# Performance work log

Hardware: AMD Instinct MI355X
Metric: run time of the kernel (lower is better)

Reference implementation:

```python
import jax, jax.numpy as jnp
import numpy as np

N = 20000        # nodes
E = 320000       # edges (avg degree 16)
IN = 128         # in_channels
D = 64           # out_channels == per-head dim (PyG TransformerConv)
H = 4            # heads
EPS_BN = 1e-5


def setup_inputs() -> dict:
    key = jax.random.key(0)
    ks = jax.random.split(key, 12)
    x = jax.random.normal(ks[0], (N, IN), jnp.float32)
    edge_index = jax.random.randint(ks[1], (2, E), 0, N, dtype=jnp.int64)
    s = 1.0 / np.sqrt(IN)
    Wq = jax.random.normal(ks[2], (IN, H * D), jnp.float32) * s
    bq = jnp.zeros((H * D,), jnp.float32)
    Wk = jax.random.normal(ks[3], (IN, H * D), jnp.float32) * s
    bk = jnp.zeros((H * D,), jnp.float32)
    Wv = jax.random.normal(ks[4], (IN, H * D), jnp.float32) * s
    bv = jnp.zeros((H * D,), jnp.float32)
    Wskip = jax.random.normal(ks[5], (IN, D), jnp.float32) * s
    bskip = jnp.zeros((D,), jnp.float32)
    gamma = jnp.ones((D,), jnp.float32)
    beta = jnp.zeros((D,), jnp.float32)
    return {"x": x, "edge_index": edge_index, "Wq": Wq, "bq": bq,
            "Wk": Wk, "bk": bk, "Wv": Wv, "bv": bv,
            "Wskip": Wskip, "bskip": bskip, "gamma": gamma, "beta": beta}


def reference(x, edge_index, Wq, bq, Wk, bk, Wv, bv, Wskip, bskip, gamma, beta):
    src = edge_index[0]   # message source j
    dst = edge_index[1]   # message target i
    # node-level projections, [N, H, D]
    q = (x @ Wq + bq).reshape(N, H, D)
    k = (x @ Wk + bk).reshape(N, H, D)
    v = (x @ Wv + bv).reshape(N, H, D)
    # per-edge attention logits [E, H]
    scores = jnp.einsum('ehd,ehd->eh', q[dst], k[src]) / jnp.sqrt(jnp.float32(D))
    # segment softmax over incoming edges of each target node
    smax = jax.ops.segment_max(scores, dst, num_segments=N)
    smax = jnp.where(jnp.isfinite(smax), smax, 0.0)  # isolated nodes
    p = jnp.exp(scores - smax[dst])
    denom = jax.ops.segment_sum(p, dst, num_segments=N)
    alpha = p / (denom[dst] + 1e-16)                  # [E, H]
    # scatter-aggregate messages: [N, H, D]
    msg = jax.ops.segment_sum(alpha[:, :, None] * v[src], dst, num_segments=N)
    # concat=False -> mean over heads; root skip connection
    out = msg.mean(axis=1) + x @ Wskip + bskip        # [N, D]
    # BatchNorm1d over nodes (training-mode batch stats, biased var)
    mu = out.mean(axis=0)
    var = out.var(axis=0)
    out = (out - mu) * jax.lax.rsqrt(var + EPS_BN) * gamma + beta
    # exact (erf) GELU, dropout = identity at eval
    return jax.nn.gelu(out, approximate=False)
```

## Files before the change

### kernel.cpp

```cpp
#include <hip/hip_runtime.h>
#include <hip/hip_fp16.h>
#include <math.h>

#define NNODES 20000
#define NEDGES 320000
#define CIN 128
#define DOUT 64
#define NHEAD 4
#define HD 256
#define PROJW 320
#define KVW 512

__global__ __launch_bounds__(256) void proj_kernel(
    const float* __restrict__ x,
    const float* __restrict__ Wq, const float* __restrict__ bq,
    const float* __restrict__ Wk, const float* __restrict__ bk,
    const float* __restrict__ Wv, const float* __restrict__ bv,
    const float* __restrict__ Ws, const float* __restrict__ bs,
    float* __restrict__ proj, __half* __restrict__ kvh)
{
    __shared__ float Ast[32][68];
    __shared__ float Bs[32][68];
    const int tile_n = blockIdx.x;
    const float* W; const float* bias; int segw; int lc0;
    if (tile_n < 4)       { W = Wq; bias = bq; segw = HD;   lc0 = tile_n * 64; }
    else if (tile_n < 8)  { W = Wk; bias = bk; segw = HD;   lc0 = (tile_n - 4) * 64; }
    else if (tile_n < 12) { W = Wv; bias = bv; segw = HD;   lc0 = (tile_n - 8) * 64; }
    else                  { W = Ws; bias = bs; segw = DOUT; lc0 = 0; }
    const int row0 = blockIdx.y * 64;
    const int tid = threadIdx.x;
    const int tx = tid & 15, ty = tid >> 4;

    float acc[4][4] = {};
    for (int k0 = 0; k0 < CIN; k0 += 32) {
        #pragma unroll
        for (int l = 0; l < 2; ++l) {
            int idx = tid + l * 256;
            int r = idx >> 3, c4 = (idx & 7) << 2;
            int gr = row0 + r;
            float4 v = make_float4(0.f, 0.f, 0.f, 0.f);
            if (gr < NNODES)
                v = *reinterpret_cast<const float4*>(x + (size_t)gr * CIN + k0 + c4);
            Ast[c4 + 0][r] = v.x; Ast[c4 + 1][r] = v.y;
            Ast[c4 + 2][r] = v.z; Ast[c4 + 3][r] = v.w;
        }
        #pragma unroll
        for (int l = 0; l < 2; ++l) {
            int idx = tid + l * 256;
            int r = idx >> 4, c4 = (idx & 15) << 2;
            float4 v = *reinterpret_cast<const float4*>(W + (size_t)(k0 + r) * segw + lc0 + c4);
            *reinterpret_cast<float4*>(&Bs[r][c4]) = v;
        }
        __syncthreads();
        #pragma unroll
        for (int kk = 0; kk < 32; ++kk) {
            const float4 a = *reinterpret_cast<const float4*>(&Ast[kk][ty * 4]);
            const float4 b = *reinterpret_cast<const float4*>(&Bs[kk][tx * 4]);
            acc[0][0] += a.x * b.x; acc[0][1] += a.x * b.y; acc[0][2] += a.x * b.z; acc[0][3] += a.x * b.w;
            acc[1][0] += a.y * b.x; acc[1][1] += a.y * b.y; acc[1][2] += a.y * b.z; acc[1][3] += a.y * b.w;
            acc[2][0] += a.z * b.x; acc[2][1] += a.z * b.y; acc[2][2] += a.z * b.z; acc[2][3] += a.z * b.w;
            acc[3][0] += a.w * b.x; acc[3][1] += a.w * b.y; acc[3][2] += a.w * b.z; acc[3][3] += a.w * b.w;
        }
        __syncthreads();
    }
    #pragma unroll
    for (int i = 0; i < 4; ++i) {
        int gr = row0 + ty * 4 + i;
        if (gr >= NNODES) continue;
        float4 o;
        o.x = acc[i][0] + bias[lc0 + tx * 4 + 0];
        o.y = acc[i][1] + bias[lc0 + tx * 4 + 1];
        o.z = acc[i][2] + bias[lc0 + tx * 4 + 2];
        o.w = acc[i][3] + bias[lc0 + tx * 4 + 3];
        if (tile_n < 4) {
            *reinterpret_cast<float4*>(proj + (size_t)gr * PROJW + tile_n * 64 + tx * 4) = o;
        } else if (tile_n < 12) {
            int col = (tile_n < 8) ? (tile_n - 4) * 64 + tx * 4
                                   : 256 + (tile_n - 8) * 64 + tx * 4;
            __half2 h0 = __floats2half2_rn(o.x, o.y);
            __half2 h1 = __floats2half2_rn(o.z, o.w);
            __half2* dst = reinterpret_cast<__half2*>(kvh + (size_t)gr * KVW + col);
            dst[0] = h0; dst[1] = h1;
        } else {
            *reinterpret_cast<float4*>(proj + (size_t)gr * PROJW + 256 + tx * 4) = o;
        }
    }
}

__global__ void hist_kernel(const int* __restrict__ ei, int* __restrict__ deg)
{
    int e = blockIdx.x * blockDim.x + threadIdx.x;
    if (e >= NEDGES) return;
    atomicAdd(&deg[ei[NEDGES + e]], 1);
}

__global__ __launch_bounds__(1024) void scan_kernel(
    const int* __restrict__ deg, int* __restrict__ rowptr, int* __restrict__ cursor)
{
    __shared__ int sd[1024];
    const int t = threadIdx.x;
    const int chunk = 20;
    const int base = t * chunk;
    int tsum = 0;
    for (int i = 0; i < chunk; ++i) {
        int idx = base + i;
        tsum += (idx < NNODES) ? deg[idx] : 0;
    }
    sd[t] = tsum; __syncthreads();
    for (int off = 1; off < 1024; off <<= 1) {
        int v = (t >= off) ? sd[t - off] : 0;
        __syncthreads();
        sd[t] += v;
        __syncthreads();
    }
    int run = sd[t] - tsum;
    for (int i = 0; i < chunk; ++i) {
        int idx = base + i;
        if (idx < NNODES) {
            int d = deg[idx];
            rowptr[idx] = run; cursor[idx] = run;
            run += d;
        }
    }
    if (t == 1023) rowptr[NNODES] = sd[1023];
}

__global__ void scatter_kernel(const int* __restrict__ ei, int* __restrict__ cursor,
                               int* __restrict__ col)
{
    int e = blockIdx.x * blockDim.x + threadIdx.x;
    if (e >= NEDGES) return;
    int src = ei[e];
    int dst = ei[NEDGES + e];
    int pos = atomicAdd(&cursor[dst], 1);
    col[pos] = src;
}

__global__ __launch_bounds__(256) void attn_kernel(
    const float* __restrict__ proj, const __half* __restrict__ kvh,
    const int* __restrict__ rowptr, const int* __restrict__ col,
    float* __restrict__ out_pre)
{
    const int node = blockIdx.x * 4 + (threadIdx.x >> 6);
    if (node >= NNODES) return;
    const int lane = threadIdx.x & 63;
    const int lane4 = lane * 4;

    const float4 q = *reinterpret_cast<const float4*>(proj + (size_t)node * PROJW + lane4);

    float m = -INFINITY, l = 0.f;
    float ax = 0.f, ay = 0.f, az = 0.f, aw = 0.f;
    int p = rowptr[node];
    const int pend = rowptr[node + 1];

    int j = (p < pend) ? col[p] : 0;
    const __half* bj = kvh + (size_t)j * KVW + lane4;
    uint2 kraw = *reinterpret_cast<const uint2*>(bj);
    uint2 vraw = *reinterpret_cast<const uint2*>(bj + 256);

    for (; p < pend; ++p) {
        const int p1 = p + 1;
        const int jn = (p1 < pend) ? col[p1] : j;
        const __half* bn = kvh + (size_t)jn * KVW + lane4;
        const uint2 krawn = *reinterpret_cast<const uint2*>(bn);
        const uint2 vrawn = *reinterpret_cast<const uint2*>(bn + 256);

        const float2 k0 = __half22float2(*reinterpret_cast<const __half2*>(&kraw.x));
        const float2 k1 = __half22float2(*reinterpret_cast<const __half2*>(&kraw.y));
        float partial = q.x * k0.x + q.y * k0.y + q.z * k1.x + q.w * k1.y;
        partial += __shfl_xor(partial, 1, 16);
        partial += __shfl_xor(partial, 2, 16);
        partial += __shfl_xor(partial, 4, 16);
        partial += __shfl_xor(partial, 8, 16);
        const float s = partial * 0.125f;
        const float mnew = fmaxf(m, s);
        const float scale = __expf(m - mnew);
        const float pc = __expf(s - mnew);
        const float2 v0 = __half22float2(*reinterpret_cast<const __half2*>(&vraw.x));
        const float2 v1 = __half22float2(*reinterpret_cast<const __half2*>(&vraw.y));
        l = l * scale + pc;
        ax = ax * scale + pc * v0.x;
        ay = ay * scale + pc * v0.y;
        az = az * scale + pc * v1.x;
        aw = aw * scale + pc * v1.y;
        m = mnew;
        kraw = krawn; vraw = vrawn;
    }
    const float inv = 1.f / (l + 1e-16f);
    float rx = ax * inv, ry = ay * inv, rz = az * inv, rw = aw * inv;
    rx += __shfl_xor(rx, 16); rx += __shfl_xor(rx, 32);
    ry += __shfl_xor(ry, 16); ry += __shfl_xor(ry, 32);
    rz += __shfl_xor(rz, 16); rz += __shfl_xor(rz, 32);
    rw += __shfl_xor(rw, 16); rw += __shfl_xor(rw, 32);
    if (lane < 16) {
        const float4 sk = *reinterpret_cast<const float4*>(proj + (size_t)node * PROJW + 256 + lane4);
        float4 o;
        o.x = rx * 0.25f + sk.x;
        o.y = ry * 0.25f + sk.y;
        o.z = rz * 0.25f + sk.z;
        o.w = rw * 0.25f + sk.w;
        *reinterpret_cast<float4*>(out_pre + (size_t)node * DOUT + lane4) = o;
    }
}

__global__ __launch_bounds__(256) void bnred_kernel(
    const float* __restrict__ out_pre, float* __restrict__ bnacc)
{
    const int tid = threadIdx.x;
    const int c = tid & 63, g = tid >> 6;
    float s = 0.f, ss = 0.f;
    for (int r = blockIdx.x * 4 + g; r < NNODES; r += gridDim.x * 4) {
        float v = out_pre[(size_t)r * DOUT + c];
        s += v; ss += v * v;
    }
    __shared__ float sd[256];
    sd[tid] = s; __syncthreads();
    float s4 = 0.f;
    if (g == 0) s4 = sd[tid] + sd[tid + 64] + sd[tid + 128] + sd[tid + 192];
    __syncthreads();
    sd[tid] = ss; __syncthreads();
    if (g == 0) {
        float ss4 = sd[tid] + sd[tid + 64] + sd[tid + 128] + sd[tid + 192];
        atomicAdd(&bnacc[c], s4);
        atomicAdd(&bnacc[64 + c], ss4);
    }
}

__global__ __launch_bounds__(256) void final_kernel(
    const float* __restrict__ out_pre, const float* __restrict__ bnacc,
    const float* __restrict__ gamma, const float* __restrict__ beta,
    float* __restrict__ out)
{
    int idx = blockIdx.x * blockDim.x + threadIdx.x;
    if (idx >= NNODES * DOUT) return;
    const int c = idx & 63;
    const float mu = bnacc[c] * (1.f / NNODES);
    const float var = bnacc[64 + c] * (1.f / NNODES) - mu * mu;
    float v = (out_pre[idx] - mu) * rsqrtf(var + 1e-5f) * gamma[c] + beta[c];
    out[idx] = v * 0.5f * (1.f + erff(v * 0.70710678118654752f));
}

extern "C" void kernel_launch(void* const* d_in, const int* in_sizes, int n_in,
                              void* d_out, int out_size, void* d_ws, size_t ws_size,
                              hipStream_t stream) {
    const float* x     = (const float*)d_in[0];
    const int*   ei    = (const int*)d_in[1];
    const float* Wq    = (const float*)d_in[2];
    const float* bq    = (const float*)d_in[3];
    const float* Wk    = (const float*)d_in[4];
    const float* bk    = (const float*)d_in[5];
    const float* Wv    = (const float*)d_in[6];
    const float* bv    = (const float*)d_in[7];
    const float* Wskip = (const float*)d_in[8];
    const float* bskip = (const float*)d_in[9];
    const float* gamma = (const float*)d_in[10];
    const float* beta  = (const float*)d_in[11];
    float* out = (float*)d_out;

    __half* kvh     = (__half*)d_ws;
    float*  proj    = (float*)((char*)d_ws + (size_t)NNODES * KVW * sizeof(__half));
    float*  out_pre = proj + (size_t)NNODES * PROJW;
    float*  bnacc   = out_pre + (size_t)NNODES * DOUT;
    int*    deg     = (int*)(bnacc + 128);
    int*    rowptr  = deg + NNODES;
    int*    cursor  = rowptr + NNODES + 1;
    int*    col     = cursor + NNODES;

    hipMemsetAsync(bnacc, 0, (128 + NNODES) * sizeof(int), stream);

    proj_kernel<<<dim3(13, (NNODES + 63) / 64), 256, 0, stream>>>(
        x, Wq, bq, Wk, bk, Wv, bv, Wskip, bskip, proj, kvh);
    hist_kernel<<<(NEDGES + 255) / 256, 256, 0, stream>>>(ei, deg);
    scan_kernel<<<1, 1024, 0, stream>>>(deg, rowptr, cursor);
    scatter_kernel<<<(NEDGES + 255) / 256, 256, 0, stream>>>(ei, cursor, col);
    attn_kernel<<<NNODES / 4, 256, 0, stream>>>(proj, kvh, rowptr, col, out_pre);
    bnred_kernel<<<128, 256, 0, stream>>>(out_pre, bnacc);
    final_kernel<<<(NNODES * DOUT + 255) / 256, 256, 0, stream>>>(
        out_pre, bnacc, gamma, beta, out);
}
```

Baseline: 277.7 us.

## Replace FP32 SIMT projection GEMM with FP16 MFMA wave-level GEMM

Adds a prep kernel that converts x to fp16 and transposes and concatenates the four weight matrices into one fp16 column-major buffer plus a combined bias. A new projection kernel has each wave compute a 16x64 output tile with mfma_f32_16x16x32_f16, replacing the LDS-tiled FP32 FMA GEMM. This moves the projection onto the matrix cores, at the cost of an extra launch, extra global traffic for the conversion, fp16 rounding of the inputs, and narrower strided scalar output stores.

```diff
diff --git a/kernel.cpp b/kernel.cpp
--- a/kernel.cpp
+++ b/kernel.cpp
@@ -10,79 +10,103 @@
 #define HD 256
 #define PROJW 320
 #define KVW 512
-
-__global__ __launch_bounds__(256) void proj_kernel(
+#define NCOL 832
+#define NWAVES (1250 * 13)
+
+typedef __attribute__((ext_vector_type(8))) _Float16 half8;
+typedef __attribute__((ext_vector_type(4))) float f32x4;
+
+__global__ __launch_bounds__(256) void prep_kernel(
     const float* __restrict__ x,
     const float* __restrict__ Wq, const float* __restrict__ bq,
     const float* __restrict__ Wk, const float* __restrict__ bk,
     const float* __restrict__ Wv, const float* __restrict__ bv,
     const float* __restrict__ Ws, const float* __restrict__ bs,
+    _Float16* __restrict__ xh, _Float16* __restrict__ Wth,
+    float* __restrict__ bias832)
+{
+    int i = blockIdx.x * 256 + threadIdx.x;
+    if (i < NNODES * CIN / 8) {
+        const float4* xv = reinterpret_cast<const float4*>(x);
+        float4 u = xv[2 * i], v = xv[2 * i + 1];
+        half8 h = { (_Float16)u.x, (_Float16)u.y, (_Float16)u.z, (_Float16)u.w,
+                    (_Float16)v.x, (_Float16)v.y, (_Float16)v.z, (_Float16)v.w };
+        *reinterpret_cast<half8*>(xh + (size_t)i * 8) = h;
+        return;
+    }
+    i -= NNODES * CIN / 8;
+    if (i < NCOL * CIN) {
+        int c = i >> 7, k = i & 127;
+        float v;
+        if (c < 256)      v = Wq[k * HD + c];
+        else if (c < 512) v = Wk[k * HD + (c - 256)];
+        else if (c < 768) v = Wv[k * HD + (c - 512)];
+        else              v = Ws[k * DOUT + (c - 768)];
+        Wth[(size_t)c * CIN + k] = (_Float16)v;
+        return;
+    }
+    i -= NCOL * CIN;
+    if (i < NCOL) {
+        float v;
+        if (i < 256)      v = bq[i];
+        else if (i < 512) v = bk[i - 256];
+        else if (i < 768) v = bv[i - 512];
+        else              v = bs[i - 768];
+        bias832[i] = v;
+    }
+}
+
+__global__ __launch_bounds__(256) void wproj_kernel(
+    const _Float16* __restrict__ xh, const _Float16* __restrict__ Wth,
+    const float* __restrict__ bias832,
     float* __restrict__ proj, __half* __restrict__ kvh)
 {
-    __shared__ float Ast[32][68];
-    __shared__ float Bs[32][68];
-    const int tile_n = blockIdx.x;
-    const float* W; const float* bias; int segw; int lc0;
-    if (tile_n < 4)       { W = Wq; bias = bq; segw = HD;   lc0 = tile_n * 64; }
-    else if (tile_n < 8)  { W = Wk; bias = bk; segw = HD;   lc0 = (tile_n - 4) * 64; }
-    else if (tile_n < 12) { W = Wv; bias = bv; segw = HD;   lc0 = (tile_n - 8) * 64; }
-    else                  { W = Ws; bias = bs; segw = DOUT; lc0 = 0; }
-    const int row0 = blockIdx.y * 64;
-    const int tid = threadIdx.x;
-    const int tx = tid & 15, ty = tid >> 4;
-
-    float acc[4][4] = {};
-    for (int k0 = 0; k0 < CIN; k0 += 32) {
-        #pragma unroll
-        for (int l = 0; l < 2; ++l) {
-            int idx = tid + l * 256;
-            int r = idx >> 3, c4 = (idx & 7) << 2;
-            int gr = row0 + r;
-            float4 v = make_float4(0.f, 0.f, 0.f, 0.f);
-            if (gr < NNODES)
-                v = *reinterpret_cast<const float4*>(x + (size_t)gr * CIN + k0 + c4);
-            Ast[c4 + 0][r] = v.x; Ast[c4 + 1][r] = v.y;
-            Ast[c4 + 2][r] = v.z; Ast[c4 + 3][r] = v.w;
-        }
-        #pragma unroll
-        for (int l = 0; l < 2; ++l) {
-            int idx = tid + l * 256;
-            int r = idx >> 4, c4 = (idx & 15) << 2;
-            float4 v = *reinterpret_cast<const float4*>(W + (size_t)(k0 + r) * segw + lc0 + c4);
-            *reinterpret_cast<float4*>(&Bs[r][c4]) = v;
-        }
-        __syncthreads();
-        #pragma unroll
-        for (int kk = 0; kk < 32; ++kk) {
-            const float4 a = *reinterpret_cast<const float4*>(&Ast[kk][ty * 4]);
-            const float4 b = *reinterpret_cast<const float4*>(&Bs[kk][tx * 4]);
-            acc[0][0] += a.x * b.x; acc[0][1] += a.x * b.y; acc[0][2] += a.x * b.z; acc[0][3] += a.x * b.w;
-            acc[1][0] += a.y * b.x; acc[1][1] += a.y * b.y; acc[1][2] += a.y * b.z; acc[1][3] += a.y * b.w;
-            acc[2][0] += a.z * b.x; acc[2][1] += a.z * b.y; acc[2][2] += a.z * b.z; acc[2][3] += a.z * b.w;
-            acc[3][0] += a.w * b.x; acc[3][1] += a.w * b.y; acc[3][2] += a.w * b.z; acc[3][3] += a.w * b.w;
-        }
-        __syncthreads();
-    }
+    const int wv = blockIdx.x * 4 + (threadIdx.x >> 6);
+    if (wv >= NWAVES) return;
+    const int l = threadIdx.x & 63;
+    const int ct = wv / 1250, rt = wv % 1250;
+    const int row0 = rt * 16, colb = ct * 64;
+    const int lrow = l & 15, lk8 = (l >> 4) * 8;
+
+    const _Float16* xr = xh + (size_t)(row0 + lrow) * CIN + lk8;
+    const half8 a0 = *reinterpret_cast<const half8*>(xr);
+    const half8 a1 = *reinterpret_cast<const half8*>(xr + 32);
+    const half8 a2 = *reinterpret_cast<const half8*>(xr + 64);
+    const half8 a3 = *reinterpret_cast<const half8*>(xr + 96);
+
+    f32x4 acc[4];
     #pragma unroll
-    for (int i = 0; i < 4; ++i) {
-        int gr = row0 + ty * 4 + i;
-        if (gr >= NNODES) continue;
-        float4 o;
-        o.x = acc[i][0] + bias[lc0 + tx * 4 + 0];
-        o.y = acc[i][1] + bias[lc0 + tx * 4 + 1];
-        o.z = acc[i][2] + bias[lc0 + tx * 4 + 2];
-        o.w = acc[i][3] + bias[lc0 + tx * 4 + 3];
-        if (tile_n < 4) {
-            *reinterpret_cast<float4*>(proj + (size_t)gr * PROJW + tile_n * 64 + tx * 4) = o;
-        } else if (tile_n < 12) {
-            int col = (tile_n < 8) ? (tile_n - 4) * 64 + tx * 4
-                                   : 256 + (tile_n - 8) * 64 + tx * 4;
-            __half2 h0 = __floats2half2_rn(o.x, o.y);
-            __half2 h1 = __floats2half2_rn(o.z, o.w);
-            __half2* dst = reinterpret_cast<__half2*>(kvh + (size_t)gr * KVW + col);
-            dst[0] = h0; dst[1] = h1;
+    for (int cg = 0; cg < 4; ++cg) {
+        const _Float16* wr = Wth + (size_t)(colb + cg * 16 + lrow) * CIN + lk8;
+        const half8 b0 = *reinterpret_cast<const half8*>(wr);
+        const half8 b1 = *reinterpret_cast<const half8*>(wr + 32);
+        const half8 b2 = *reinterpret_cast<const half8*>(wr + 64);
+        const half8 b3 = *reinterpret_cast<const half8*>(wr + 96);
+        f32x4 c = {0.f, 0.f, 0.f, 0.f};
+        c = __builtin_amdgcn_mfma_f32_16x16x32_f16(a0, b0, c, 0, 0, 0);
+        c = __builtin_amdgcn_mfma_f32_16x16x32_f16(a1, b1, c, 0, 0, 0);
+        c = __builtin_amdgcn_mfma_f32_16x16x32_f16(a2, b2, c, 0, 0, 0);
+        c = __builtin_amdgcn_mfma_f32_16x16x32_f16(a3, b3, c, 0, 0, 0);
+        acc[cg] = c;
+    }
+
+    const int orow = row0 + (l >> 4) * 4;
+    #pragma unroll
+    for (int cg = 0; cg < 4; ++cg) {
+        const int c = colb + cg * 16 + lrow;
+        const float bias = bias832[c];
+        if (ct < 4) {
+            #pragma unroll
+            for (int r = 0; r < 4; ++r)
+                proj[(size_t)(orow + r) * PROJW + c] = acc[cg][r] + bias;
+        } else if (ct < 12) {
+            #pragma unroll
+            for (int r = 0; r < 4; ++r)
+                kvh[(size_t)(orow + r) * KVW + (c - 256)] = __float2half(acc[cg][r] + bias);
         } else {
-            *reinterpret_cast<float4*>(proj + (size_t)gr * PROJW + 256 + tx * 4) = o;
+            #pragma unroll
+            for (int r = 0; r < 4; ++r)
+                proj[(size_t)(orow + r) * PROJW + (c - 512)] = acc[cg][r] + bias;
         }
     }
 }
@@ -257,19 +281,24 @@
     const float* beta  = (const float*)d_in[11];
     float* out = (float*)d_out;
 
-    __half* kvh     = (__half*)d_ws;
-    float*  proj    = (float*)((char*)d_ws + (size_t)NNODES * KVW * sizeof(__half));
-    float*  out_pre = proj + (size_t)NNODES * PROJW;
-    float*  bnacc   = out_pre + (size_t)NNODES * DOUT;
-    int*    deg     = (int*)(bnacc + 128);
-    int*    rowptr  = deg + NNODES;
-    int*    cursor  = rowptr + NNODES + 1;
-    int*    col     = cursor + NNODES;
+    __half*   kvh    = (__half*)d_ws;
+    _Float16* xh     = (_Float16*)((char*)d_ws + 20480000);
+    _Float16* Wth    = xh + (size_t)NNODES * CIN;
+    float*    bias832= (float*)(Wth + (size_t)NCOL * CIN);
+    float*    proj   = bias832 + NCOL;
+    float*    out_pre= proj + (size_t)NNODES * PROJW;
+    float*    bnacc  = out_pre + (size_t)NNODES * DOUT;
+    int*      deg    = (int*)(bnacc + 128);
+    int*      rowptr = deg + NNODES;
+    int*      cursor = rowptr + NNODES + 1;
+    int*      col    = cursor + NNODES;
 
     hipMemsetAsync(bnacc, 0, (128 + NNODES) * sizeof(int), stream);
 
-    proj_kernel<<<dim3(13, (NNODES + 63) / 64), 256, 0, stream>>>(
-        x, Wq, bq, Wk, bk, Wv, bv, Wskip, bskip, proj, kvh);
+    const int prep_total = NNODES * CIN / 8 + NCOL * CIN + NCOL;
+    prep_kernel<<<(prep_total + 255) / 256, 256, 0, stream>>>(
+        x, Wq, bq, Wk, bk, Wv, bv, Wskip, bskip, xh, Wth, bias832);
+    wproj_kernel<<<(NWAVES + 3) / 4, 256, 0, stream>>>(xh, Wth, bias832, proj, kvh);
     hist_kernel<<<(NEDGES + 255) / 256, 256, 0, stream>>>(ei, deg);
     scan_kernel<<<1, 1024, 0, stream>>>(deg, rowptr, cursor);
     scatter_kernel<<<(NEDGES + 255) / 256, 256, 0, stream>>>(ei, cursor, col);
```

Result: faster. 264.6 us (-4.7%).
